# Kernel tuning notes

Measured on AMD Instinct MI355X. Metric: run time of the kernel, lower is better.

Reference implementation:

```python
import jax, jax.numpy as jnp
import numpy as np

SENS = 200
DM = 128
NMAPS = 2
NLAYERS = 2
TH = 0.01
EPS = 1e-5
BATCH = 8
SEQ = 96
HEADS = 8


def setup_inputs() -> dict:
    key = jax.random.key(0)
    ks = jax.random.split(key, 8)
    x = jax.random.normal(ks[0], (BATCH, SENS, SEQ, DM), jnp.float32)
    attn_s = jax.random.uniform(ks[1], (1, BATCH, HEADS, SENS, SENS), jnp.float32)
    supports = jax.random.uniform(ks[2], (SENS, SENS), jnp.float32)
    W_conv = jax.random.normal(ks[3], (NMAPS, NLAYERS, DM, DM), jnp.float32) * 0.05
    b_conv = jnp.zeros((NMAPS, NLAYERS, DM), jnp.float32)
    bn_gamma = jnp.ones((NMAPS, DM), jnp.float32)
    bn_beta = jnp.zeros((NMAPS, DM), jnp.float32)
    W_out = jax.random.normal(ks[4], (NMAPS * DM, DM), jnp.float32) * 0.05
    b_out = jnp.zeros((DM,), jnp.float32)
    return dict(x=x, attn_s=attn_s, supports=supports, W_conv=W_conv,
                b_conv=b_conv, bn_gamma=bn_gamma, bn_beta=bn_beta,
                W_out=W_out, b_out=b_out)


def _process_map(A):
    # make_symmetric: lower triangle + mirrored strict lower triangle
    A = jnp.tril(A) + jnp.tril(A, -1).T
    # clamp: threshold on absolute value; note original returns |A| thresholded
    Aa = jnp.abs(A)
    A = jnp.where(Aa > TH, Aa, jnp.zeros_like(Aa))
    # SparseTensor.from_dense(A).t()
    return A.T


def _gcn_norm(adj_t):
    # GCNConv default: add self-loops (weight 1), symmetric D^-1/2 A D^-1/2
    A = adj_t + jnp.eye(adj_t.shape[0], dtype=adj_t.dtype)
    deg = A.sum(axis=1)
    d = jnp.where(deg > 0, jax.lax.rsqrt(deg), jnp.zeros_like(deg))
    return d[:, None] * A * d[None, :]


def reference(x, attn_s, supports, W_conv, b_conv, bn_gamma, bn_beta, W_out, b_out):
    B, N, S, D = x.shape
    # reshape_mat: [B,N,S,D] -> [B*S, N, D]
    xr = x.transpose(0, 2, 1, 3).reshape(B * S, N, D)

    # supports: [data map, adaptive map from attention (mean over batch, heads)]
    maps = [_process_map(supports), _process_map(attn_s[0].mean(axis=(0, 1)))]

    gcn_outputs = []
    for i in range(NMAPS):
        An = _gcn_norm(maps[i])  # [N,N]
        h = jnp.zeros_like(xr[..., :1]) * 0.0  # placeholder replaced below
        h = None
        for l in range(NLAYERS):
            xw = jnp.einsum('bnf,fg->bng', xr, W_conv[i, l])
            hl = jnp.einsum('mn,bng->bmg', An, xw) + b_conv[i, l]
            h = hl if h is None else h + hl
        # BatchNorm1d over feature channel (training-mode batch stats, biased var)
        mu = h.mean(axis=(0, 1))
        var = h.var(axis=(0, 1))
        hn = (h - mu) * jax.lax.rsqrt(var + EPS) * bn_gamma[i] + bn_beta[i]
        gcn_outputs.append(jax.nn.relu(hn))

    cat = jnp.concatenate(gcn_outputs, axis=-1)  # [B*S, N, NMAPS*DM]
    y = jax.nn.relu(jnp.einsum('bnc,cd->bnd', cat, W_out) + b_out)
    # inverse_reshape_mat: [B*S, N, D] -> [B, N, S, D]
    return y.reshape(B, S, N, D).transpose(0, 2, 1, 3)
```

## Files before the change

kernel.cpp:

```cpp
#include <hip/hip_runtime.h>

#define SENS 200
#define DM 128
#define SEQ 96
#define BS 768
#define NTOT 153600
#define TH 0.01f
#define BN_EPS 1e-5f
#define MPAD 224
#define KP 208
#define XSS 132
#define ASROW 68

typedef __attribute__((ext_vector_type(8)))  __bf16 bf16x8;
typedef __attribute__((ext_vector_type(4)))  __bf16 bf16x4;
typedef __attribute__((ext_vector_type(16))) float  f32x16;

__device__ __forceinline__ f32x16 mfma32(bf16x8 a, bf16x8 b, f32x16 c) {
    return __builtin_amdgcn_mfma_f32_32x32x16_bf16(a, b, c, 0, 0, 0);
}
__device__ __forceinline__ bf16x8 join8(bf16x4 a, bf16x4 b) {
    bf16x8 r;
    #pragma unroll
    for (int j = 0; j < 4; ++j) { r[j] = a[j]; r[j + 4] = b[j]; }
    return r;
}
__device__ __forceinline__ unsigned pk2(float a, float b) {
    union { unsigned u; __bf16 hh[2]; } t;
    t.hh[0] = (__bf16)a; t.hh[1] = (__bf16)b;
    return t.u;
}
__device__ __forceinline__ void permswap(unsigned &a, unsigned &b) {
    asm("v_permlane32_swap_b32 %0, %1" : "+v"(a), "+v"(b));
}
__device__ __forceinline__ bf16x8 frag4(unsigned a, unsigned b, unsigned c, unsigned d) {
    union { unsigned u[4]; bf16x8 v; } t;
    t.u[0] = a; t.u[1] = b; t.u[2] = c; t.u[3] = d;
    return t.v;
}

__global__ void attn_mean_kernel(const float* __restrict__ attn, float* __restrict__ mapA) {
    int idx = blockIdx.x * 256 + threadIdx.x;
    if (idx >= SENS * SENS) return;
    float s = 0.f;
    #pragma unroll 8
    for (int q = 0; q < 64; ++q) s += attn[(size_t)q * SENS * SENS + idx];
    mapA[idx] = s * (1.0f / 64.0f);
}

__global__ void build_map_kernel(const float* __restrict__ supports, const float* __restrict__ mapA,
                                 float* __restrict__ M, float* __restrict__ deg) {
    __shared__ float red[256];
    int m = blockIdx.x, map = blockIdx.y, j = threadIdx.x;
    const float* src = (map == 0) ? supports : mapA;
    float v = 0.f;
    if (j < SENS) {
        float sym = (m >= j) ? src[m * SENS + j] : src[j * SENS + m];
        float a = fabsf(sym);
        v = (a > TH) ? a : 0.f;
        M[(size_t)map * SENS * SENS + m * SENS + j] = v;
    }
    red[j] = v;
    __syncthreads();
    for (int off = 128; off > 0; off >>= 1) {
        if (j < off) red[j] += red[j + off];
        __syncthreads();
    }
    if (j == 0) deg[map * SENS + m] = red[0] + 1.0f;
}

__global__ __launch_bounds__(256) void prep2_kernel(
    const float* __restrict__ M, const float* __restrict__ deg,
    const float* __restrict__ W_conv, const float* __restrict__ b_conv,
    const float* __restrict__ W_out,
    __bf16* __restrict__ Anb, __bf16* __restrict__ Wt, __bf16* __restrict__ Wot,
    float* __restrict__ bsum, float* __restrict__ bnacc)
{
    const int bid = blockIdx.x, t = threadIdx.x;
    if (bid < 2 * MPAD) {
        const int map = bid / MPAD, m = bid % MPAD;
        const int j = t;
        if (j < KP) {
            float val = 0.f;
            if (m < SENS && j < SENS) {
                float a = M[((size_t)map * SENS + m) * SENS + j] + ((m == j) ? 1.f : 0.f);
                val = rsqrtf(deg[map * SENS + m]) * a * rsqrtf(deg[map * SENS + j]);
            }
            Anb[(((size_t)map * 13 + (j >> 4)) * MPAD + m) * 16 + (j & 15)] = (__bf16)val;
        }
    } else {
        const int idx = (bid - 2 * MPAD) * 256 + t;
        if (idx < 32768) {
            const int map = idx >> 14, g = (idx >> 7) & 127, f = idx & 127;
            const float* wp = W_conv + (size_t)map * 2 * DM * DM + f * DM + g;
            Wt[(((size_t)map * 8 + (f >> 4)) * DM + g) * 16 + (f & 15)] = (__bf16)(wp[0] + wp[DM * DM]);
        } else if (idx < 65536) {
            const int k = idx - 32768, d = k >> 8, c = k & 255;
            Wot[(((size_t)(c >> 4)) * DM + d) * 16 + (c & 15)] = (__bf16)W_out[c * DM + d];
        } else if (idx < 65792) {
            const int k = idx - 65536, map = k >> 7, g = k & 127;
            bsum[k] = b_conv[(map * 2) * DM + g] + b_conv[(map * 2 + 1) * DM + g];
        } else if (idx < 66304) {
            bnacc[idx - 65792] = 0.f;
        }
    }
}

__global__ __launch_bounds__(256, 2) void conv_kernel(
    const float* __restrict__ x, const __bf16* __restrict__ Anb,
    const __bf16* __restrict__ Wt, const float* __restrict__ bsum,
    __bf16* __restrict__ h, float* __restrict__ bnacc)
{
    __shared__ __bf16 xs[MPAD * XSS];
    const int bs = blockIdx.x;
    const int b = bs / SEQ, s = bs % SEQ;
    const int t = threadIdx.x;
    const int wt = t >> 6, lane = t & 63;
    const int l31 = lane & 31, hi = lane >> 5;

    {
        const float* xb = x + ((size_t)b * SENS * SEQ + s) * DM;
        for (int i = t; i < SENS * 32; i += 256) {
            const int n = i >> 5, c = i & 31;
            const float4 v = *(const float4*)(xb + (size_t)n * SEQ * DM + c * 4);
            union { uint2 u; __bf16 hh[4]; } p;
            p.hh[0] = (__bf16)v.x; p.hh[1] = (__bf16)v.y;
            p.hh[2] = (__bf16)v.z; p.hh[3] = (__bf16)v.w;
            *(uint2*)(&xs[n * XSS + c * 4]) = p.u;
        }
        unsigned* zp = (unsigned*)(&xs[SENS * XSS]);
        for (int i = t; i < (MPAD - SENS) * (XSS / 2); i += 256) zp[i] = 0u;
    }
    __syncthreads();

    #pragma unroll 1
    for (int map = 0; map < 2; ++map) {
        bf16x8 wf[8];
        {
            const __bf16* wb = Wt + (((size_t)map * 8) * DM + wt * 32 + l31) * 16 + hi * 8;
            #pragma unroll
            for (int k = 0; k < 8; ++k) wf[k] = *(const bf16x8*)(wb + (size_t)k * DM * 16);
        }
        bf16x8 xwf[13];
        #pragma unroll
        for (int nt = 0; nt < 7; ++nt) {
            f32x16 acc;
            #pragma unroll
            for (int r = 0; r < 16; ++r) acc[r] = 0.f;
            const __bf16* xp = &xs[(nt * 32 + l31) * XSS + hi * 8];
            #pragma unroll
            for (int k = 0; k < 8; ++k)
                acc = mfma32(*(const bf16x8*)(xp + k * 16), wf[k], acc);
            {
                unsigned w0 = pk2(acc[0], acc[1]),  w1 = pk2(acc[2], acc[3]);
                unsigned w2 = pk2(acc[4], acc[5]),  w3 = pk2(acc[6], acc[7]);
                permswap(w0, w2); permswap(w1, w3);
                xwf[2 * nt] = frag4(w0, w1, w2, w3);
            }
            if (nt < 6) {
                unsigned w0 = pk2(acc[8], acc[9]),   w1 = pk2(acc[10], acc[11]);
                unsigned w2 = pk2(acc[12], acc[13]), w3 = pk2(acc[14], acc[15]);
                permswap(w0, w2); permswap(w1, w3);
                xwf[2 * nt + 1] = frag4(w0, w1, w2, w3);
            }
        }

        f32x16 acc2[7];
        #pragma unroll
        for (int mt = 0; mt < 7; ++mt)
            #pragma unroll
            for (int r = 0; r < 16; ++r) acc2[mt][r] = 0.f;
        {
            const __bf16* ab = Anb + (((size_t)map * 13) * MPAD + l31) * 16 + hi * 8;
            #pragma unroll
            for (int kc = 0; kc < 13; ++kc) {
                #pragma unroll
                for (int mt = 0; mt < 7; ++mt) {
                    const bf16x8 af = *(const bf16x8*)(ab + ((size_t)kc * MPAD + mt * 32) * 16);
                    acc2[mt] = mfma32(af, xwf[kc], acc2[mt]);
                }
            }
        }

        const float bias = bsum[map * DM + wt * 32 + l31];
        float sv = 0.f, qv = 0.f;
        #pragma unroll
        for (int mt = 0; mt < 7; ++mt) {
            bf16x8 h0, h1;
            #pragma unroll
            for (int r = 0; r < 16; ++r) {
                const float v = acc2[mt][r] + bias;
                if (r < 8) h0[r] = (__bf16)v; else h1[r - 8] = (__bf16)v;
                const int m = mt * 32 + (r & 3) + 8 * (r >> 2) + 4 * hi;
                if (m < SENS) { sv += v; qv += v * v; }
            }
            __bf16* hp = h + ((((size_t)(bs * 2 + map) * 7 + mt) * 4 + wt) * 64 + lane) * 16;
            *(bf16x8*)hp = h0;
            *(bf16x8*)(hp + 8) = h1;
        }
        sv += __shfl_xor(sv, 32);
        qv += __shfl_xor(qv, 32);
        if (hi == 0) {
            atomicAdd(&bnacc[map * DM + wt * 32 + l31], sv);
            atomicAdd(&bnacc[256 + map * DM + wt * 32 + l31], qv);
        }
    }
}

__device__ __forceinline__ void out_stage(int cn, int t, int bs,
                                          const __bf16* __restrict__ h,
                                          const float* sc_s, const float* sh_s,
                                          __bf16* dst)
{
    const int mapn = cn >> 1;
    const __bf16* hb = h + ((size_t)(bs * 2 + mapn) * 28 + (cn & 1) * 2) * 1024;
    bf16x8 vv[4];
    #pragma unroll
    for (int it = 0; it < 4; ++it) {
        const int idx = it * 512 + t;
        if (idx < 1792)
            vv[it] = *(const bf16x8*)(hb + ((size_t)(idx >> 8) * 4 + ((idx >> 7) & 1)) * 1024
                                          + ((idx >> 1) & 63) * 16 + (idx & 1) * 8);
    }
    #pragma unroll
    for (int it = 0; it < 4; ++it) {
        const int idx = it * 512 + t;
        if (idx < 1792) {
            const int half = idx & 1, lane_s = (idx >> 1) & 63;
            const int ctl = (idx >> 7) & 1, strip = idx >> 8;
            const int cl = ctl * 32 + (lane_s & 31);
            const int cg = mapn * DM + (cn & 1) * 64 + cl;
            const float scv = sc_s[cg], shv = sh_s[cg];
            const int mbase = strip * 32 + 4 * (lane_s >> 5) + 16 * half;
            #pragma unroll
            for (int q2 = 0; q2 < 8; ++q2) {
                const int row = mbase + (q2 & 3) + 8 * (q2 >> 2);
                const float fv = (float)vv[it][q2] * scv + shv;
                dst[row * ASROW + cl] = (__bf16)fmaxf(fv, 0.f);
            }
        }
    }
}

__global__ __launch_bounds__(512) void out_kernel(
    const __bf16* __restrict__ h, const __bf16* __restrict__ Wot,
    const float* __restrict__ bnacc,
    const float* __restrict__ gamma, const float* __restrict__ beta,
    const float* __restrict__ b_out, float* __restrict__ out)
{
    __shared__ __bf16 As[2][MPAD * ASROW];
    __shared__ float sc_s[256], sh_s[256];
    const int bs = blockIdx.x;
    const int b = bs / SEQ, s = bs % SEQ;
    const int t = threadIdx.x, w = t >> 6, lane = t & 63;
    const int l31 = lane & 31, hi = lane >> 5;
    const int dct = w & 3, sbase = w >> 2;
    if (t < 256) {
        const float mu = bnacc[t] * (1.f / (float)NTOT);
        const float var = bnacc[256 + t] * (1.f / (float)NTOT) - mu * mu;
        const float sc = gamma[t] * rsqrtf(var + BN_EPS);
        sc_s[t] = sc;
        sh_s[t] = beta[t] - mu * sc;
    }
    f32x16 acc[4];
    {
        const float bo = b_out[dct * 32 + l31];
        #pragma unroll
        for (int i = 0; i < 4; ++i)
            #pragma unroll
            for (int r = 0; r < 16; ++r) acc[i][r] = bo;
    }
    __syncthreads();
    out_stage(0, t, bs, h, sc_s, sh_s, &As[0][0]);
    __syncthreads();
    for (int c = 0; c < 4; ++c) {
        #pragma unroll
        for (int kc = 0; kc < 4; ++kc) {
            bf16x8 bfrag = *(const bf16x8*)(Wot + ((size_t)(c * 4 + kc) * DM + dct * 32 + l31) * 16 + hi * 8);
            #pragma unroll
            for (int i = 0; i < 4; ++i) {
                const int strip = sbase + 2 * i;
                if (strip >= 7) break;
                const __bf16* ap = &As[c & 1][(strip * 32 + l31) * ASROW + kc * 16 + hi * 8];
                acc[i] = mfma32(join8(*(const bf16x4*)ap, *(const bf16x4*)(ap + 4)), bfrag, acc[i]);
            }
        }
        if (c < 3) out_stage(c + 1, t, bs, h, sc_s, sh_s, &As[(c + 1) & 1][0]);
        __syncthreads();
    }
    #pragma unroll
    for (int i = 0; i < 4; ++i) {
        const int strip = sbase + 2 * i;
        if (strip >= 7) break;
        #pragma unroll
        for (int r = 0; r < 16; ++r) {
            const int m = strip * 32 + (r & 3) + 8 * (r >> 2) + 4 * hi;
            if (m < SENS)
                out[(((size_t)b * SENS + m) * SEQ + s) * DM + dct * 32 + l31] = fmaxf(acc[i][r], 0.f);
        }
    }
}

extern "C" void kernel_launch(void* const* d_in, const int* in_sizes, int n_in,
                              void* d_out, int out_size, void* d_ws, size_t ws_size,
                              hipStream_t stream) {
    const float* x        = (const float*)d_in[0];
    const float* attn     = (const float*)d_in[1];
    const float* supports = (const float*)d_in[2];
    const float* W_conv   = (const float*)d_in[3];
    const float* b_conv   = (const float*)d_in[4];
    const float* gamma    = (const float*)d_in[5];
    const float* beta     = (const float*)d_in[6];
    const float* W_out    = (const float*)d_in[7];
    const float* b_out    = (const float*)d_in[8];
    float* out = (float*)d_out;
    char* base = (char*)d_ws;

    float*  mapA  = (float*)(base + 0);
    float*  Mbuf  = (float*)(base + 160000);
    float*  deg   = (float*)(base + 480000);
    float*  bnacc = (float*)(base + 481664);
    float*  bsum  = (float*)(base + 483712);
    __bf16* Wt    = (__bf16*)(base + 484736);
    __bf16* Wot   = (__bf16*)(base + 550272);
    __bf16* Anb   = (__bf16*)(base + 615808);
    __bf16* h     = (__bf16*)(base + 1048576);

    attn_mean_kernel<<<157, 256, 0, stream>>>(attn, mapA);
    build_map_kernel<<<dim3(SENS, 2), 256, 0, stream>>>(supports, mapA, Mbuf, deg);
    prep2_kernel<<<2 * MPAD + 260, 256, 0, stream>>>(Mbuf, deg, W_conv, b_conv, W_out,
                                                     Anb, Wt, Wot, bsum, bnacc);
    conv_kernel<<<BS, 256, 0, stream>>>(x, Anb, Wt, bsum, h, bnacc);
    out_kernel<<<BS, 512, 0, stream>>>(h, Wot, bnacc, gamma, beta, b_out, out);
}
```

Before: 276.8 us.

## Split conv kernel maps across 8 waves and chunk the aggregation accumulators

The conv kernel now launches 512 threads per block, and each group of four waves handles one of the two adjacency maps concurrently instead of looping over the maps sequentially. The second GEMM's seven output tiles are split into chunks of four and three accumulators to reduce register pressure, paired with launch bounds of 512 threads and 4 blocks. This is meant to raise wave-level parallelism and occupancy. The cost is possible register spills under the tighter bound, and the shared-memory tile now serves more waves per block.

New measurement: 325.2 us. +17.5%, slower.

```diff
diff --git a/kernel.cpp b/kernel.cpp
--- a/kernel.cpp
+++ b/kernel.cpp
@@ -106,7 +106,7 @@
     }
 }
 
-__global__ __launch_bounds__(256, 2) void conv_kernel(
+__global__ __launch_bounds__(512, 4) void conv_kernel(
     const float* __restrict__ x, const __bf16* __restrict__ Anb,
     const __bf16* __restrict__ Wt, const float* __restrict__ bsum,
     __bf16* __restrict__ h, float* __restrict__ bnacc)
@@ -115,12 +115,13 @@
     const int bs = blockIdx.x;
     const int b = bs / SEQ, s = bs % SEQ;
     const int t = threadIdx.x;
-    const int wt = t >> 6, lane = t & 63;
+    const int w = t >> 6, lane = t & 63;
+    const int map = w >> 2, gt = w & 3;
     const int l31 = lane & 31, hi = lane >> 5;
 
     {
         const float* xb = x + ((size_t)b * SENS * SEQ + s) * DM;
-        for (int i = t; i < SENS * 32; i += 256) {
+        for (int i = t; i < SENS * 32; i += 512) {
             const int n = i >> 5, c = i & 31;
             const float4 v = *(const float4*)(xb + (size_t)n * SEQ * DM + c * 4);
             union { uint2 u; __bf16 hh[4]; } p;
@@ -129,19 +130,16 @@
             *(uint2*)(&xs[n * XSS + c * 4]) = p.u;
         }
         unsigned* zp = (unsigned*)(&xs[SENS * XSS]);
-        for (int i = t; i < (MPAD - SENS) * (XSS / 2); i += 256) zp[i] = 0u;
+        for (int i = t; i < (MPAD - SENS) * (XSS / 2); i += 512) zp[i] = 0u;
     }
     __syncthreads();
 
-    #pragma unroll 1
-    for (int map = 0; map < 2; ++map) {
+    bf16x8 xwf[13];
+    {
         bf16x8 wf[8];
-        {
-            const __bf16* wb = Wt + (((size_t)map * 8) * DM + wt * 32 + l31) * 16 + hi * 8;
-            #pragma unroll
-            for (int k = 0; k < 8; ++k) wf[k] = *(const bf16x8*)(wb + (size_t)k * DM * 16);
-        }
-        bf16x8 xwf[13];
+        const __bf16* wb = Wt + (((size_t)map * 8) * DM + gt * 32 + l31) * 16 + hi * 8;
+        #pragma unroll
+        for (int k = 0; k < 8; ++k) wf[k] = *(const bf16x8*)(wb + (size_t)k * DM * 16);
         #pragma unroll
         for (int nt = 0; nt < 7; ++nt) {
             f32x16 acc;
@@ -164,46 +162,77 @@
                 xwf[2 * nt + 1] = frag4(w0, w1, w2, w3);
             }
         }
-
-        f32x16 acc2[7];
-        #pragma unroll
-        for (int mt = 0; mt < 7; ++mt)
-            #pragma unroll
-            for (int r = 0; r < 16; ++r) acc2[mt][r] = 0.f;
-        {
-            const __bf16* ab = Anb + (((size_t)map * 13) * MPAD + l31) * 16 + hi * 8;
-            #pragma unroll
-            for (int kc = 0; kc < 13; ++kc) {
-                #pragma unroll
-                for (int mt = 0; mt < 7; ++mt) {
-                    const bf16x8 af = *(const bf16x8*)(ab + ((size_t)kc * MPAD + mt * 32) * 16);
-                    acc2[mt] = mfma32(af, xwf[kc], acc2[mt]);
-                }
-            }
-        }
-
-        const float bias = bsum[map * DM + wt * 32 + l31];
-        float sv = 0.f, qv = 0.f;
-        #pragma unroll
-        for (int mt = 0; mt < 7; ++mt) {
+    }
+
+    const float bias = bsum[map * DM + gt * 32 + l31];
+    float sv = 0.f, qv = 0.f;
+    const __bf16* abase = Anb + (((size_t)map * 13) * MPAD + l31) * 16 + hi * 8;
+
+    {
+        f32x16 acc2[4];
+        #pragma unroll
+        for (int mi = 0; mi < 4; ++mi)
+            #pragma unroll
+            for (int r = 0; r < 16; ++r) acc2[mi][r] = 0.f;
+        #pragma unroll
+        for (int kc = 0; kc < 13; ++kc) {
+            const __bf16* ap = abase + (size_t)kc * MPAD * 16;
+            #pragma unroll
+            for (int mi = 0; mi < 4; ++mi)
+                acc2[mi] = mfma32(*(const bf16x8*)(ap + mi * 32 * 16), xwf[kc], acc2[mi]);
+        }
+        #pragma unroll
+        for (int mi = 0; mi < 4; ++mi) {
+            const int mt = mi;
             bf16x8 h0, h1;
             #pragma unroll
             for (int r = 0; r < 16; ++r) {
-                const float v = acc2[mt][r] + bias;
+                const float v = acc2[mi][r] + bias;
                 if (r < 8) h0[r] = (__bf16)v; else h1[r - 8] = (__bf16)v;
                 const int m = mt * 32 + (r & 3) + 8 * (r >> 2) + 4 * hi;
                 if (m < SENS) { sv += v; qv += v * v; }
             }
-            __bf16* hp = h + ((((size_t)(bs * 2 + map) * 7 + mt) * 4 + wt) * 64 + lane) * 16;
+            __bf16* hp = h + ((((size_t)(bs * 2 + map) * 7 + mt) * 4 + gt) * 64 + lane) * 16;
             *(bf16x8*)hp = h0;
             *(bf16x8*)(hp + 8) = h1;
         }
-        sv += __shfl_xor(sv, 32);
-        qv += __shfl_xor(qv, 32);
-        if (hi == 0) {
-            atomicAdd(&bnacc[map * DM + wt * 32 + l31], sv);
-            atomicAdd(&bnacc[256 + map * DM + wt * 32 + l31], qv);
-        }
+    }
+
+    {
+        f32x16 acc2[3];
+        #pragma unroll
+        for (int mi = 0; mi < 3; ++mi)
+            #pragma unroll
+            for (int r = 0; r < 16; ++r) acc2[mi][r] = 0.f;
+        #pragma unroll
+        for (int kc = 0; kc < 13; ++kc) {
+            const __bf16* ap = abase + ((size_t)kc * MPAD + 4 * 32) * 16;
+            #pragma unroll
+            for (int mi = 0; mi < 3; ++mi)
+                acc2[mi] = mfma32(*(const bf16x8*)(ap + mi * 32 * 16), xwf[kc], acc2[mi]);
+        }
+        #pragma unroll
+        for (int mi = 0; mi < 3; ++mi) {
+            const int mt = 4 + mi;
+            bf16x8 h0, h1;
+            #pragma unroll
+            for (int r = 0; r < 16; ++r) {
+                const float v = acc2[mi][r] + bias;
+                if (r < 8) h0[r] = (__bf16)v; else h1[r - 8] = (__bf16)v;
+                const int m = mt * 32 + (r & 3) + 8 * (r >> 2) + 4 * hi;
+                if (m < SENS) { sv += v; qv += v * v; }
+            }
+            __bf16* hp = h + ((((size_t)(bs * 2 + map) * 7 + mt) * 4 + gt) * 64 + lane) * 16;
+            *(bf16x8*)hp = h0;
+            *(bf16x8*)(hp + 8) = h1;
+        }
+    }
+
+    sv += __shfl_xor(sv, 32);
+    qv += __shfl_xor(qv, 32);
+    if (hi == 0) {
+        atomicAdd(&bnacc[map * DM + gt * 32 + l31], sv);
+        atomicAdd(&bnacc[256 + map * DM + gt * 32 + l31], qv);
     }
 }
 
@@ -330,6 +359,6 @@
     build_map_kernel<<<dim3(SENS, 2), 256, 0, stream>>>(supports, mapA, Mbuf, deg);
     prep2_kernel<<<2 * MPAD + 260, 256, 0, stream>>>(Mbuf, deg, W_conv, b_conv, W_out,
                                                      Anb, Wt, Wot, bsum, bnacc);
-    conv_kernel<<<BS, 256, 0, stream>>>(x, Anb, Wt, bsum, h, bnacc);
+    conv_kernel<<<BS, 512, 0, stream>>>(x, Anb, Wt, bsum, h, bnacc);
     out_kernel<<<BS, 512, 0, stream>>>(h, Wot, bnacc, gamma, beta, b_out, out);
 }
```
